# Kernel tuning notes

Hardware: AMD Instinct MI355X
Metric: run time of the kernel (lower is better)

## Reference

```python
import jax, jax.numpy as jnp
import numpy as np

N, E, D_IN, D_H = 20000, 320000, 512, 512
ALPHA = 0.1
LAMBDA = 1.0

def setup_inputs() -> dict:
    key = jax.random.key(0)
    ks = jax.random.split(key, 12)
    feat = jax.random.normal(ks[0], (N, D_IN), dtype=jnp.float32)
    src = jax.random.randint(ks[1], (E,), 0, N, dtype=jnp.int32)
    dst = jax.random.randint(ks[2], (E,), 0, N, dtype=jnp.int32)
    s = 0.05
    fc_w = jax.random.normal(ks[3], (D_H, D_IN), dtype=jnp.float32) * s  # torch Linear: [out,in]
    fc_b = jax.random.normal(ks[4], (D_H,), dtype=jnp.float32) * s
    w1_1 = jax.random.normal(ks[5], (D_H, D_H), dtype=jnp.float32) * s
    w2_1 = jax.random.normal(ks[6], (D_H, D_H), dtype=jnp.float32) * s
    b_1 = jax.random.normal(ks[7], (D_H,), dtype=jnp.float32) * s
    w1_2 = jax.random.normal(ks[8], (D_H, D_H), dtype=jnp.float32) * s
    w2_2 = jax.random.normal(ks[9], (D_H, D_H), dtype=jnp.float32) * s
    b_2 = jax.random.normal(ks[10], (D_H,), dtype=jnp.float32) * s
    return {"feat": feat, "src": src, "dst": dst, "fc_w": fc_w, "fc_b": fc_b,
            "w1_1": w1_1, "w2_1": w2_1, "b_1": b_1,
            "w1_2": w1_2, "w2_2": w2_2, "b_2": b_2}


def _gcn2_layer(h, h0, src, dst, norm, w1, w2, b, layer):
    # DGL GCN2Conv (project_initial_features=False)
    beta = float(np.log(LAMBDA / layer + 1.0))
    x = h * norm                      # [N, D]
    agg = jax.ops.segment_sum(x[src], dst, num_segments=h.shape[0])  # SpMM: sum over in-neighbors
    agg = agg * norm
    f = agg * (1.0 - ALPHA)
    f0 = h0 * ALPHA
    rst = ((1.0 - beta) * f + beta * (f @ w1)
           + (1.0 - beta) * f0 + beta * (f0 @ w2) + b)
    return jax.nn.relu(rst)


def reference(feat, src, dst, fc_w, fc_b, w1_1, w2_1, b_1, w1_2, w2_2, b_2):
    n = feat.shape[0]
    h = feat @ fc_w.T + fc_b          # initial projection
    # symmetric norm from in-degrees (clamped at 1), as in DGL
    deg = jax.ops.segment_sum(jnp.ones_like(dst, dtype=h.dtype), dst, num_segments=n)
    norm = jnp.clip(deg, 1.0, None) ** -0.5
    norm = norm[:, None]
    res = _gcn2_layer(h, h, src, dst, norm, w1_1, w2_1, b_1, layer=1)
    out = _gcn2_layer(res, h, src, dst, norm, w1_2, w2_2, b_2, layer=2)
    return out
```

## Files before the change

kernel.cpp:

```cpp
#include <hip/hip_runtime.h>
#include <hip/hip_bf16.h>
#include <stdint.h>
#include <stddef.h>

typedef __bf16 bf16_t;
typedef __bf16 bf16x4 __attribute__((ext_vector_type(4)));
typedef __bf16 bf16x8 __attribute__((ext_vector_type(8)));
typedef float floatx4 __attribute__((ext_vector_type(4)));

#define NN 20000
#define EE 320000
#define DD 512
#define CAP 96
#define BETA1 0.6931471805599453f
#define BETA2 0.40546510810816444f

__device__ __forceinline__ void gload16(const bf16_t* g, bf16_t* l) {
  __builtin_amdgcn_global_load_lds((const __attribute__((address_space(1))) uint32_t*)g,
                                   (__attribute__((address_space(3))) uint32_t*)l, 16, 0, 0);
}

__global__ void bucket_kernel(const int* __restrict__ src, const int* __restrict__ dst,
                              int* __restrict__ cnt, int* __restrict__ esrc, int E) {
  int e = blockIdx.x * 256 + threadIdx.x;
  if (e < E) {
    int d = dst[e];
    int pos = atomicAdd(&cnt[d], 1);
    if (pos < CAP) esrc[d * CAP + pos] = src[e];
  }
}

__global__ void norm_kernel(const int* __restrict__ cnt, float* __restrict__ nrm, int n) {
  int i = blockIdx.x * 256 + threadIdx.x;
  if (i < n) nrm[i] = 1.0f / sqrtf(fmaxf((float)cnt[i], 1.0f));
}

__global__ void cvt_kernel(const float* __restrict__ in, bf16_t* __restrict__ out, int n4) {
  int i = blockIdx.x * 256 + threadIdx.x;
  if (i < n4) {
    float4 v = ((const float4*)in)[i];
    bf16x4 o = {(bf16_t)v.x, (bf16_t)v.y, (bf16_t)v.z, (bf16_t)v.w};
    ((bf16x4*)out)[i] = o;
  }
}

__global__ void transpose_cat(const float* __restrict__ W1, const float* __restrict__ W2,
                              bf16_t* __restrict__ BT, int K) {
  __shared__ bf16_t tile[32][33];
  int k0 = blockIdx.y * 32;
  int n0 = blockIdx.x * 32;
  int tx = threadIdx.x, ty = threadIdx.y;
  const float* W = (k0 < 512) ? W1 : W2;
  int kk = (k0 < 512) ? k0 : (k0 - 512);
#pragma unroll
  for (int i = 0; i < 32; i += 8)
    tile[ty + i][tx] = (bf16_t)W[(size_t)(kk + ty + i) * 512 + n0 + tx];
  __syncthreads();
#pragma unroll
  for (int i = 0; i < 32; i += 8)
    BT[(size_t)(n0 + ty + i) * K + k0 + tx] = tile[tx][ty + i];
}

__global__ __launch_bounds__(256) void aggregate_kernel(
    const bf16_t* __restrict__ hin, const float* __restrict__ nrm,
    const int* __restrict__ cnt, const int* __restrict__ esrc,
    bf16_t* __restrict__ Acat) {
  int node = blockIdx.x * 4 + (threadIdx.x >> 6);
  if (node >= NN) return;
  int lane = threadIdx.x & 63;
  const int* eb = esrc + (size_t)node * CAP;
  int n_e = cnt[node];
  n_e = n_e < CAP ? n_e : CAP;

  float acc[8] = {};
  bf16x8 v0 = {}, v1 = {}, v2 = {}, v3 = {};
  float ns0 = 0, ns1 = 0, ns2 = 0, ns3 = 0;

#define LOADJ(j, idx)                                                  \
  {                                                                    \
    int s = eb[idx];                                                   \
    ns##j = nrm[s];                                                    \
    v##j = *(const bf16x8*)(hin + (size_t)s * DD + lane * 8);          \
  }

  if (0 < n_e) LOADJ(0, 0)
  if (1 < n_e) LOADJ(1, 1)
  if (2 < n_e) LOADJ(2, 2)
  if (3 < n_e) LOADJ(3, 3)

  for (int i = 0; i < n_e; i += 4) {
    {
      bf16x8 a = v0; float na = ns0;
      if (i + 4 < n_e) LOADJ(0, i + 4)
#pragma unroll
      for (int k = 0; k < 8; ++k) acc[k] += na * (float)a[k];
    }
    if (i + 1 < n_e) {
      bf16x8 a = v1; float na = ns1;
      if (i + 5 < n_e) LOADJ(1, i + 5)
#pragma unroll
      for (int k = 0; k < 8; ++k) acc[k] += na * (float)a[k];
    }
    if (i + 2 < n_e) {
      bf16x8 a = v2; float na = ns2;
      if (i + 6 < n_e) LOADJ(2, i + 6)
#pragma unroll
      for (int k = 0; k < 8; ++k) acc[k] += na * (float)a[k];
    }
    if (i + 3 < n_e) {
      bf16x8 a = v3; float na = ns3;
      if (i + 7 < n_e) LOADJ(3, i + 7)
#pragma unroll
      for (int k = 0; k < 8; ++k) acc[k] += na * (float)a[k];
    }
  }
#undef LOADJ

  float nd = 0.9f * nrm[node];
  bf16x8 ob;
#pragma unroll
  for (int k = 0; k < 8; ++k) ob[k] = (bf16_t)(nd * acc[k]);
  *(bf16x8*)(Acat + (size_t)node * 1024 + lane * 8) = ob;
}

template <int MODE>
__global__ __launch_bounds__(256) void gemm_kernel(
    const bf16_t* __restrict__ A, const bf16_t* __restrict__ BT,
    int lda, int ldb, int K, int M,
    const float* __restrict__ bias,
    const bf16_t* __restrict__ acat_ro, float beta,
    float* __restrict__ outf, bf16_t* __restrict__ outb,
    bf16_t* __restrict__ acat2) {
  __shared__ bf16_t As[2][64 * 32];
  __shared__ bf16_t Bs[2][128 * 32];

  const int bid = blockIdx.x;
  const int mt = (bid >> 5) * 8 + (bid & 7);
  const int nt = (bid >> 3) & 3;
  const int m0 = mt * 64;
  if (m0 >= M) return;
  const int n0 = nt * 128;

  const int t = threadIdx.x;
  const int lane = t & 63;
  const int w = t >> 6;
  const int wm = w & 1, wn = w >> 1;
  const int quad = lane >> 4, m16 = lane & 15;

  const int r0 = t >> 2;
  const int kc = (t & 3) ^ ((r0 >> 1) & 3);
  int arow_g = m0 + r0; arow_g = arow_g < M ? arow_g : M - 1;
  const bf16_t* agp  = A  + (size_t)arow_g * lda + kc * 8;
  const bf16_t* bgp0 = BT + (size_t)(n0 + r0) * ldb + kc * 8;
  const bf16_t* bgp1 = BT + (size_t)(n0 + 64 + r0) * ldb + kc * 8;

  floatx4 acc[2][4] = {};
  const int niter = K >> 5;

  gload16(agp,  &As[0][t * 8]);
  gload16(bgp0, &Bs[0][t * 8]);
  gload16(bgp1, &Bs[0][(t + 256) * 8]);

  for (int kt = 0; kt < niter; ++kt) {
    __syncthreads();
    const int b = kt & 1;
    if (kt + 1 < niter) {
      const int nb = b ^ 1;
      const int ko = (kt + 1) * 32;
      gload16(agp + ko,  &As[nb][t * 8]);
      gload16(bgp0 + ko, &Bs[nb][t * 8]);
      gload16(bgp1 + ko, &Bs[nb][(t + 256) * 8]);
    }

    bf16x8 af[2], bfr[4];
#pragma unroll
    for (int i = 0; i < 2; ++i) {
      int arow = wm * 32 + i * 16 + m16;
      int ac = quad ^ ((arow >> 1) & 3);
      af[i] = *(const bf16x8*)(&As[b][(arow * 4 + ac) * 8]);
    }
#pragma unroll
    for (int j = 0; j < 4; ++j) {
      int brow = wn * 64 + j * 16 + m16;
      int bc = quad ^ ((brow >> 1) & 3);
      bfr[j] = *(const bf16x8*)(&Bs[b][(brow * 4 + bc) * 8]);
    }
#pragma unroll
    for (int i = 0; i < 2; ++i)
#pragma unroll
      for (int j = 0; j < 4; ++j)
        acc[i][j] = __builtin_amdgcn_mfma_f32_16x16x32_bf16(af[i], bfr[j], acc[i][j], 0, 0, 0);
  }

#pragma unroll
  for (int i = 0; i < 2; ++i) {
#pragma unroll
    for (int j = 0; j < 4; ++j) {
      int col = n0 + wn * 64 + j * 16 + m16;
      float bv = bias[col];
#pragma unroll
      for (int p = 0; p < 4; ++p) {
        int row = m0 + wm * 32 + i * 16 + quad * 4 + p;
        if (row < M) {
          size_t idx = (size_t)row * DD + col;
          float v = acc[i][j][p];
          if constexpr (MODE == 0) {
            float hv = v + bv;
            outb[idx] = (bf16_t)hv;
            acat2[(size_t)row * 1024 + 512 + col] = (bf16_t)(0.1f * hv);
          } else {
            float fsv = (float)acat_ro[(size_t)row * 1024 + col] +
                        (float)acat_ro[(size_t)row * 1024 + 512 + col];
            float r = (1.0f - beta) * fsv + beta * v + bv;
            r = fmaxf(r, 0.0f);
            if constexpr (MODE == 1) outb[idx] = (bf16_t)r;
            else outf[idx] = r;
          }
        }
      }
    }
  }
}

extern "C" void kernel_launch(void* const* d_in, const int* in_sizes, int n_in,
                              void* d_out, int out_size, void* d_ws, size_t ws_size,
                              hipStream_t stream) {
  const float* feat = (const float*)d_in[0];
  const int* src = (const int*)d_in[1];
  const int* dst = (const int*)d_in[2];
  const float* fc_w = (const float*)d_in[3];
  const float* fc_b = (const float*)d_in[4];
  const float* w1_1 = (const float*)d_in[5];
  const float* w2_1 = (const float*)d_in[6];
  const float* b_1  = (const float*)d_in[7];
  const float* w1_2 = (const float*)d_in[8];
  const float* w2_2 = (const float*)d_in[9];
  const float* b_2  = (const float*)d_in[10];
  float* out = (float*)d_out;

  char* ws = (char*)d_ws;
  size_t off = 0;
  auto alloc = [&](size_t bytes) {
    char* p = ws + off;
    off += (bytes + 255) & ~(size_t)255;
    return p;
  };
  const size_t NDf = (size_t)NN * DD;
  bf16_t* h_bf   = (bf16_t*)alloc(NDf * sizeof(bf16_t));
  bf16_t* res_bf = (bf16_t*)alloc(NDf * sizeof(bf16_t));
  bf16_t* featb  = (bf16_t*)alloc(NDf * sizeof(bf16_t));
  bf16_t* Acat   = (bf16_t*)alloc((size_t)NN * 1024 * sizeof(bf16_t));
  bf16_t* BW0    = (bf16_t*)alloc((size_t)512 * 512 * sizeof(bf16_t));
  bf16_t* BT1    = (bf16_t*)alloc((size_t)512 * 1024 * sizeof(bf16_t));
  bf16_t* BT2    = (bf16_t*)alloc((size_t)512 * 1024 * sizeof(bf16_t));
  int*    cnt    = (int*)alloc((size_t)NN * sizeof(int));
  float*  nrm    = (float*)alloc((size_t)NN * sizeof(float));
  int*    esrc   = (int*)alloc((size_t)NN * CAP * sizeof(int));

  hipMemsetAsync(cnt, 0, (size_t)NN * sizeof(int), stream);
  bucket_kernel<<<(EE + 255) / 256, 256, 0, stream>>>(src, dst, cnt, esrc, EE);
  norm_kernel<<<(NN + 255) / 256, 256, 0, stream>>>(cnt, nrm, NN);

  cvt_kernel<<<(int)(NDf / 4 / 256), 256, 0, stream>>>(feat, featb, (int)(NDf / 4));
  cvt_kernel<<<(512 * 512 / 4) / 256, 256, 0, stream>>>(fc_w, BW0, 512 * 512 / 4);

  transpose_cat<<<dim3(16, 32), dim3(32, 8), 0, stream>>>(w1_1, w2_1, BT1, 1024);
  transpose_cat<<<dim3(16, 32), dim3(32, 8), 0, stream>>>(w1_2, w2_2, BT2, 1024);

  const int gblocks = 1280;

  gemm_kernel<0><<<gblocks, 256, 0, stream>>>(featb, BW0, 512, 512, 512, NN, fc_b,
                                              nullptr, 0.0f, nullptr, h_bf, Acat);

  aggregate_kernel<<<(NN + 3) / 4, 256, 0, stream>>>(h_bf, nrm, cnt, esrc, Acat);
  gemm_kernel<1><<<gblocks, 256, 0, stream>>>(Acat, BT1, 1024, 1024, 1024, NN, b_1,
                                              Acat, BETA1, nullptr, res_bf, nullptr);

  aggregate_kernel<<<(NN + 3) / 4, 256, 0, stream>>>(res_bf, nrm, cnt, esrc, Acat);
  gemm_kernel<2><<<gblocks, 256, 0, stream>>>(Acat, BT2, 1024, 1024, 1024, NN, b_2,
                                              Acat, BETA2, out, nullptr, nullptr);
}
```

Before: 379.9 us.

## Replace LDS-staged GEMM with direct-to-register loads and larger 128x128 tiles

The GEMM kernel drops its shared-memory double buffer filled by global_load_lds and instead has each wave load its MFMA fragments straight from global memory into registers, ping-ponging two register sets across k-steps. The block tile grows from 64x128 to 128x128 (each wave now computes 64x64 with a 4x4 accumulator array), and the grid is halved. The aim is to remove LDS traffic and the per-iteration barrier. In exchange there is no cross-wave sharing of loaded tiles, so global/L2 traffic per MFMA rises, register pressure grows, and the 16-byte row-strided loads are less coalesced.

```diff
diff --git a/kernel.cpp b/kernel.cpp
--- a/kernel.cpp
+++ b/kernel.cpp
@@ -14,11 +14,6 @@
 #define CAP 96
 #define BETA1 0.6931471805599453f
 #define BETA2 0.40546510810816444f
-
-__device__ __forceinline__ void gload16(const bf16_t* g, bf16_t* l) {
-  __builtin_amdgcn_global_load_lds((const __attribute__((address_space(1))) uint32_t*)g,
-                                   (__attribute__((address_space(3))) uint32_t*)l, 16, 0, 0);
-}
 
 __global__ void bucket_kernel(const int* __restrict__ src, const int* __restrict__ dst,
                               int* __restrict__ cnt, int* __restrict__ esrc, int E) {
@@ -131,13 +126,10 @@
     const bf16_t* __restrict__ acat_ro, float beta,
     float* __restrict__ outf, bf16_t* __restrict__ outb,
     bf16_t* __restrict__ acat2) {
-  __shared__ bf16_t As[2][64 * 32];
-  __shared__ bf16_t Bs[2][128 * 32];
-
   const int bid = blockIdx.x;
   const int mt = (bid >> 5) * 8 + (bid & 7);
   const int nt = (bid >> 3) & 3;
-  const int m0 = mt * 64;
+  const int m0 = mt * 128;
   if (m0 >= M) return;
   const int n0 = nt * 128;
 
@@ -147,60 +139,58 @@
   const int wm = w & 1, wn = w >> 1;
   const int quad = lane >> 4, m16 = lane & 15;
 
-  const int r0 = t >> 2;
-  const int kc = (t & 3) ^ ((r0 >> 1) & 3);
-  int arow_g = m0 + r0; arow_g = arow_g < M ? arow_g : M - 1;
-  const bf16_t* agp  = A  + (size_t)arow_g * lda + kc * 8;
-  const bf16_t* bgp0 = BT + (size_t)(n0 + r0) * ldb + kc * 8;
-  const bf16_t* bgp1 = BT + (size_t)(n0 + 64 + r0) * ldb + kc * 8;
-
-  floatx4 acc[2][4] = {};
+  const bf16_t* ap[4];
+  const bf16_t* bp[4];
+#pragma unroll
+  for (int i = 0; i < 4; ++i) {
+    int arow = m0 + wm * 64 + i * 16 + m16;
+    arow = arow < M ? arow : M - 1;
+    ap[i] = A + (size_t)arow * lda + quad * 8;
+    bp[i] = BT + (size_t)(n0 + wn * 64 + i * 16 + m16) * ldb + quad * 8;
+  }
+
+  floatx4 acc[4][4] = {};
   const int niter = K >> 5;
 
-  gload16(agp,  &As[0][t * 8]);
-  gload16(bgp0, &Bs[0][t * 8]);
-  gload16(bgp1, &Bs[0][(t + 256) * 8]);
-
-  for (int kt = 0; kt < niter; ++kt) {
-    __syncthreads();
-    const int b = kt & 1;
-    if (kt + 1 < niter) {
-      const int nb = b ^ 1;
-      const int ko = (kt + 1) * 32;
-      gload16(agp + ko,  &As[nb][t * 8]);
-      gload16(bgp0 + ko, &Bs[nb][t * 8]);
-      gload16(bgp1 + ko, &Bs[nb][(t + 256) * 8]);
-    }
-
-    bf16x8 af[2], bfr[4];
-#pragma unroll
-    for (int i = 0; i < 2; ++i) {
-      int arow = wm * 32 + i * 16 + m16;
-      int ac = quad ^ ((arow >> 1) & 3);
-      af[i] = *(const bf16x8*)(&As[b][(arow * 4 + ac) * 8]);
-    }
-#pragma unroll
-    for (int j = 0; j < 4; ++j) {
-      int brow = wn * 64 + j * 16 + m16;
-      int bc = quad ^ ((brow >> 1) & 3);
-      bfr[j] = *(const bf16x8*)(&Bs[b][(brow * 4 + bc) * 8]);
-    }
-#pragma unroll
-    for (int i = 0; i < 2; ++i)
-#pragma unroll
-      for (int j = 0; j < 4; ++j)
-        acc[i][j] = __builtin_amdgcn_mfma_f32_16x16x32_bf16(af[i], bfr[j], acc[i][j], 0, 0, 0);
-  }
-
-#pragma unroll
-  for (int i = 0; i < 2; ++i) {
+  bf16x8 a0[4], b0[4], a1[4], b1[4];
+#define LOADSET(as, bs, kt)                                       \
+  {                                                               \
+    const int ko = (kt) * 32;                                     \
+    _Pragma("unroll")                                             \
+    for (int i = 0; i < 4; ++i) {                                 \
+      as[i] = *(const bf16x8*)(ap[i] + ko);                       \
+      bs[i] = *(const bf16x8*)(bp[i] + ko);                       \
+    }                                                             \
+  }
+#define MFMASET(as, bs)                                           \
+  {                                                               \
+    _Pragma("unroll")                                             \
+    for (int i = 0; i < 4; ++i)                                   \
+      _Pragma("unroll")                                           \
+      for (int j = 0; j < 4; ++j)                                 \
+        acc[i][j] = __builtin_amdgcn_mfma_f32_16x16x32_bf16(      \
+            as[i], bs[j], acc[i][j], 0, 0, 0);                    \
+  }
+
+  LOADSET(a0, b0, 0)
+  for (int kt = 0; kt < niter; kt += 2) {
+    if (kt + 1 < niter) LOADSET(a1, b1, kt + 1)
+    MFMASET(a0, b0)
+    if (kt + 2 < niter) LOADSET(a0, b0, kt + 2)
+    if (kt + 1 < niter) MFMASET(a1, b1)
+  }
+#undef LOADSET
+#undef MFMASET
+
+#pragma unroll
+  for (int i = 0; i < 4; ++i) {
 #pragma unroll
     for (int j = 0; j < 4; ++j) {
       int col = n0 + wn * 64 + j * 16 + m16;
       float bv = bias[col];
 #pragma unroll
       for (int p = 0; p < 4; ++p) {
-        int row = m0 + wm * 32 + i * 16 + quad * 4 + p;
+        int row = m0 + wm * 64 + i * 16 + quad * 4 + p;
         if (row < M) {
           size_t idx = (size_t)row * DD + col;
           float v = acc[i][j][p];
@@ -267,7 +257,7 @@
   transpose_cat<<<dim3(16, 32), dim3(32, 8), 0, stream>>>(w1_1, w2_1, BT1, 1024);
   transpose_cat<<<dim3(16, 32), dim3(32, 8), 0, stream>>>(w1_2, w2_2, BT2, 1024);
 
-  const int gblocks = 1280;
+  const int gblocks = 640;
 
   gemm_kernel<0><<<gblocks, 256, 0, stream>>>(featb, BW0, 512, 512, 512, NN, fc_b,
                                               nullptr, 0.0f, nullptr, h_bf, Acat);
```

Measured after the change: 516.5 us. 36.0% more time.
